# Kernel optimization log

Measured on AMD Instinct MI355X. Metric: run time of the kernel, lower is better.

## Reference

```python
import jax, jax.numpy as jnp
import numpy as np

EPS_RMS = 1e-6  # mmfreelm RMSNorm default eps

def _rmsnorm(x, w):
    var = jnp.mean(x * x, axis=-1, keepdims=True)
    return x * jax.lax.rsqrt(var + EPS_RMS) * w

def _activation_quant(x):
    # per-token absmax int8 quant (BitNet b1.58 activation quant)
    scale = 127.0 / jnp.clip(jnp.max(jnp.abs(x), axis=-1, keepdims=True), 1e-5)
    return jnp.clip(jnp.round(x * scale), -128.0, 127.0) / scale

def _weight_quant(w):
    # ternary quant with global mean-abs scale
    scale = 1.0 / jnp.clip(jnp.mean(jnp.abs(w)), 1e-5)
    return jnp.clip(jnp.round(w * scale), -1.0, 1.0) / scale

def _nm_mask(w, n, m):
    # keep top-n by |w| in every group of m along the input (last) dim
    O, I = w.shape
    g = jnp.abs(w).reshape(-1, m)            # [G, m]
    _, idx = jax.lax.top_k(g, n)             # [G, n]
    rows = jnp.arange(g.shape[0])[:, None]
    mask = jnp.zeros_like(g).at[rows, idx].set(1.0)
    return mask.reshape(O, I)

def setup_inputs() -> dict:
    key = jax.random.key(0)
    k1, k2 = jax.random.split(key)
    B, S, IN, OUT = 4, 2048, 4096, 11008
    x = jax.random.normal(k1, (B, S, IN), dtype=jnp.float32)
    weight = jax.random.normal(k2, (OUT, IN), dtype=jnp.float32) * 0.02
    norm_weight = jnp.ones((IN,), dtype=jnp.float32)
    return {"x": x, "weight": weight, "norm_weight": norm_weight,
            "sparse_n": 2, "sparse_m": 4}

def reference(x, weight, norm_weight, sparse_n, sparse_m):
    x_norm = _rmsnorm(x, norm_weight)
    # STE quantization (forward value == quantized value)
    x_q = x_norm + jax.lax.stop_gradient(_activation_quant(x_norm) - x_norm)
    w_q = weight + jax.lax.stop_gradient(_weight_quant(weight) - weight)
    mask = jax.lax.stop_gradient(_nm_mask(w_q, sparse_n, sparse_m))
    w_sparse = w_q * mask                    # [OUT, IN]
    return jnp.einsum('bsi,oi->bso', x_q, w_sparse)
```

## Files before the change

### kernel.cpp

```cpp
#include <hip/hip_runtime.h>
#include <stdint.h>

#define IN_DIM 4096
#define OUT_DIM 11008
#define TOKENS 8192
#define WN (45088768L)

typedef int int4v __attribute__((ext_vector_type(4)));

__device__ __forceinline__ float bf2f(uint32_t u16) {
  union { uint32_t i; float f; } v; v.i = u16 << 16; return v.f;
}
__device__ __forceinline__ bool probe_bf16(const void* nw) {
  return ((const uint16_t*)nw)[0] == 0x3F80u;
}

__global__ __launch_bounds__(256) void k_wabs(const void* __restrict__ wv,
                                              const void* __restrict__ nwv,
                                              double* __restrict__ partial) {
  const bool b16 = probe_bf16(nwv);
  const long tid = (long)blockIdx.x * 256 + threadIdx.x;
  const long stride = (long)gridDim.x * 256;
  double s = 0.0;
  if (b16) {
    const uint4* w = (const uint4*)wv;
    for (long i = tid; i < WN / 8; i += stride) {
      uint4 v = w[i];
      uint32_t a[4] = {v.x, v.y, v.z, v.w};
      float t = 0.f;
#pragma unroll
      for (int j = 0; j < 4; j++)
        t += fabsf(bf2f(a[j] & 0xffffu)) + fabsf(bf2f(a[j] >> 16));
      s += (double)t;
    }
  } else {
    const float4* w = (const float4*)wv;
    for (long i = tid; i < WN / 4; i += stride) {
      float4 v = w[i];
      s += (double)(fabsf(v.x) + fabsf(v.y) + fabsf(v.z) + fabsf(v.w));
    }
  }
#pragma unroll
  for (int off = 32; off > 0; off >>= 1) s += __shfl_down(s, off);
  __shared__ double sd[4];
  if ((threadIdx.x & 63) == 0) sd[threadIdx.x >> 6] = s;
  __syncthreads();
  if (threadIdx.x == 0) partial[blockIdx.x] = (sd[0] + sd[1]) + (sd[2] + sd[3]);
}

__global__ __launch_bounds__(256) void k_wscale(const double* __restrict__ partial,
                                                float* __restrict__ hdr) {
  double s = 0.0;
  for (int i = threadIdx.x; i < 2048; i += 256) s += partial[i];
#pragma unroll
  for (int off = 32; off > 0; off >>= 1) s += __shfl_down(s, off);
  __shared__ double sd[4];
  if ((threadIdx.x & 63) == 0) sd[threadIdx.x >> 6] = s;
  __syncthreads();
  if (threadIdx.x == 0) {
    double mean = ((sd[0] + sd[1]) + (sd[2] + sd[3])) / (double)WN;
    float meanc = (float)mean;
    if (meanc < 1e-5f) meanc = 1e-5f;
    float wscale = 1.0f / meanc;
    hdr[0] = wscale;
    hdr[1] = 1.0f / wscale;
  }
}

__global__ __launch_bounds__(256) void k_act(const void* __restrict__ xv,
                                             const void* __restrict__ nwv,
                                             int8_t* __restrict__ qx,
                                             float* __restrict__ invsx) {
  const bool b16 = probe_bf16(nwv);
  const int t = blockIdx.x;
  const int tx = threadIdx.x;
  float xw[16];
  float ss = 0.f, mx = 0.f;
  if (b16) {
    const uint16_t* xr = (const uint16_t*)xv + (long)t * IN_DIM;
    const uint16_t* nw = (const uint16_t*)nwv;
#pragma unroll
    for (int c = 0; c < 2; c++) {
      uint4 vx = ((const uint4*)xr)[tx * 2 + c];
      uint4 vn = ((const uint4*)nw)[tx * 2 + c];
      uint32_t ax[4] = {vx.x, vx.y, vx.z, vx.w};
      uint32_t an[4] = {vn.x, vn.y, vn.z, vn.w};
#pragma unroll
      for (int j = 0; j < 4; j++) {
        float x0 = bf2f(ax[j] & 0xffffu), x1 = bf2f(ax[j] >> 16);
        float n0 = bf2f(an[j] & 0xffffu), n1 = bf2f(an[j] >> 16);
        ss += x0 * x0 + x1 * x1;
        float p0 = x0 * n0, p1 = x1 * n1;
        xw[c * 8 + j * 2]     = p0;
        xw[c * 8 + j * 2 + 1] = p1;
        mx = fmaxf(mx, fmaxf(fabsf(p0), fabsf(p1)));
      }
    }
  } else {
    const float* xr = (const float*)xv + (long)t * IN_DIM;
    const float* nw = (const float*)nwv;
#pragma unroll
    for (int c = 0; c < 4; c++) {
      float4 vx = ((const float4*)xr)[tx * 4 + c];
      float4 vn = ((const float4*)nw)[tx * 4 + c];
      ss += vx.x * vx.x + vx.y * vx.y + vx.z * vx.z + vx.w * vx.w;
      float p0 = vx.x * vn.x, p1 = vx.y * vn.y, p2 = vx.z * vn.z, p3 = vx.w * vn.w;
      xw[c * 4 + 0] = p0; xw[c * 4 + 1] = p1; xw[c * 4 + 2] = p2; xw[c * 4 + 3] = p3;
      mx = fmaxf(mx, fmaxf(fmaxf(fabsf(p0), fabsf(p1)), fmaxf(fabsf(p2), fabsf(p3))));
    }
  }
#pragma unroll
  for (int off = 32; off > 0; off >>= 1) {
    ss += __shfl_down(ss, off);
    mx = fmaxf(mx, __shfl_down(mx, off));
  }
  __shared__ float s_ss[4], s_mx[4];
  __shared__ float bc[1];
  if ((tx & 63) == 0) { s_ss[tx >> 6] = ss; s_mx[tx >> 6] = mx; }
  __syncthreads();
  if (tx == 0) {
    float sst = (s_ss[0] + s_ss[1]) + (s_ss[2] + s_ss[3]);
    float mxt = fmaxf(fmaxf(s_mx[0], s_mx[1]), fmaxf(s_mx[2], s_mx[3]));
    float var = sst / (float)IN_DIM;
    float rms = 1.0f / sqrtf(var + 1e-6f);
    float amax = rms * mxt;
    if (amax < 1e-5f) amax = 1e-5f;
    float scale = 127.0f / amax;
    bc[0] = rms * scale;
    invsx[t] = 1.0f / scale;
  }
  __syncthreads();
  float rsc = bc[0];
  uint32_t pw[4];
#pragma unroll
  for (int d = 0; d < 4; d++) {
    uint32_t v = 0;
#pragma unroll
    for (int j = 0; j < 4; j++) {
      float q = rintf(xw[d * 4 + j] * rsc);
      q = fminf(fmaxf(q, -128.f), 127.f);
      int qi = (int)q;
      v |= ((uint32_t)(qi & 0xff)) << (8 * j);
    }
    pw[d] = v;
  }
  uint4 st; st.x = pw[0]; st.y = pw[1]; st.z = pw[2]; st.w = pw[3];
  ((uint4*)(qx + (long)t * IN_DIM))[tx] = st;
}

__global__ __launch_bounds__(256) void k_wq(const void* __restrict__ wv,
                                            const void* __restrict__ nwv,
                                            const float* __restrict__ hdr,
                                            int8_t* __restrict__ qw) {
  const bool b16 = probe_bf16(nwv);
  const long i = (long)blockIdx.x * 256 + threadIdx.x;
  const float wscale = hdr[0];
  float f[8];
  if (b16) {
    uint4 v = ((const uint4*)wv)[i];
    uint32_t a[4] = {v.x, v.y, v.z, v.w};
#pragma unroll
    for (int j = 0; j < 4; j++) {
      f[j * 2]     = bf2f(a[j] & 0xffffu);
      f[j * 2 + 1] = bf2f(a[j] >> 16);
    }
  } else {
    float4 v0 = ((const float4*)wv)[i * 2];
    float4 v1 = ((const float4*)wv)[i * 2 + 1];
    f[0] = v0.x; f[1] = v0.y; f[2] = v0.z; f[3] = v0.w;
    f[4] = v1.x; f[5] = v1.y; f[6] = v1.z; f[7] = v1.w;
  }
  int q[8];
#pragma unroll
  for (int j = 0; j < 8; j++) {
    float qf = rintf(f[j] * wscale);
    qf = fminf(fmaxf(qf, -1.f), 1.f);
    q[j] = (int)qf;
  }
#pragma unroll
  for (int g = 0; g < 2; g++) {
    int cnt = 0;
#pragma unroll
    for (int j = 0; j < 4; j++) {
      int idx = g * 4 + j;
      if (q[idx] != 0) { cnt++; if (cnt > 2) q[idx] = 0; }
    }
  }
  uint32_t lo = 0, hi = 0;
#pragma unroll
  for (int j = 0; j < 4; j++) lo |= ((uint32_t)(q[j] & 0xff)) << (8 * j);
#pragma unroll
  for (int j = 0; j < 4; j++) hi |= ((uint32_t)(q[4 + j] & 0xff)) << (8 * j);
  uint2 st; st.x = lo; st.y = hi;
  ((uint2*)qw)[i] = st;
}

__global__ __launch_bounds__(256) void k_gemm(const int8_t* __restrict__ qx,
                                              const int8_t* __restrict__ qw,
                                              const float* __restrict__ invsx,
                                              const float* __restrict__ hdr,
                                              float* __restrict__ out) {
  __shared__ __align__(16) int8_t sA[128 * 64];
  __shared__ __align__(16) int8_t sB[128 * 64];
  const int tx = threadIdx.x;
  const int wave = tx >> 6, lane = tx & 63;
  const int wr = wave >> 1, wc = wave & 1;
  const int m0 = blockIdx.y * 128, n0 = blockIdx.x * 128;

  const int rowA  = tx >> 2;
  const int col16 = (tx & 3) * 16;
  const int8_t* gA = qx + (long)(m0 + rowA) * IN_DIM + col16;
  const int8_t* gB = qw + (long)(n0 + rowA) * IN_DIM + col16;
  int8_t* lA = sA + wave * 1024;
  int8_t* lB = sB + wave * 1024;

  const int kb = (lane >> 4) * 16;
  const int lr = lane & 15;
  const int8_t* pa[4];
  const int8_t* pb[4];
#pragma unroll
  for (int m = 0; m < 4; m++) pa[m] = sA + (wr * 64 + m * 16 + lr) * 64 + kb;
#pragma unroll
  for (int n = 0; n < 4; n++) pb[n] = sB + (wc * 64 + n * 16 + lr) * 64 + kb;

  int4v zero = {0, 0, 0, 0};
  int4v acc[4][4];
#pragma unroll
  for (int m = 0; m < 4; m++)
#pragma unroll
    for (int n = 0; n < 4; n++) acc[m][n] = zero;

  for (int kt = 0; kt < IN_DIM; kt += 64) {
#pragma unroll
    for (int ph = 0; ph < 2; ph++) {
      __builtin_amdgcn_global_load_lds(
          (const __attribute__((address_space(1))) void*)(gA + (long)ph * 64 * IN_DIM + kt),
          (__attribute__((address_space(3))) void*)(lA + ph * 4096), 16, 0, 0);
      __builtin_amdgcn_global_load_lds(
          (const __attribute__((address_space(1))) void*)(gB + (long)ph * 64 * IN_DIM + kt),
          (__attribute__((address_space(3))) void*)(lB + ph * 4096), 16, 0, 0);
    }
    __syncthreads();
    int4v a[4], b[4];
#pragma unroll
    for (int m = 0; m < 4; m++) a[m] = *(const int4v*)pa[m];
#pragma unroll
    for (int n = 0; n < 4; n++) b[n] = *(const int4v*)pb[n];
#pragma unroll
    for (int m = 0; m < 4; m++)
#pragma unroll
      for (int n = 0; n < 4; n++)
        acc[m][n] = __builtin_amdgcn_mfma_i32_16x16x64_i8(a[m], b[n], acc[m][n], 0, 0, 0);
    __syncthreads();
  }

  const float winv = hdr[1];
#pragma unroll
  for (int m = 0; m < 4; m++) {
    const int rbase = m0 + wr * 64 + m * 16 + (lane >> 4) * 4;
#pragma unroll
    for (int r = 0; r < 4; r++) {
      const int trow = rbase + r;
      const float fs = invsx[trow] * winv;
      const long ob = (long)trow * OUT_DIM + n0 + wc * 64 + lr;
#pragma unroll
      for (int n = 0; n < 4; n++) {
        out[ob + n * 16] = (float)acc[m][n][r] * fs;
      }
    }
  }
}

extern "C" void kernel_launch(void* const* d_in, const int* in_sizes, int n_in,
                              void* d_out, int out_size, void* d_ws, size_t ws_size,
                              hipStream_t stream) {
  const void* x  = d_in[0];
  const void* w  = d_in[1];
  const void* nw = d_in[2];
  float* out = (float*)d_out;

  char* ws = (char*)d_ws;
  float*  hdr     = (float*)ws;
  double* partial = (double*)(ws + 1024);
  float*  invsx   = (float*)(ws + 20480);
  int8_t* qx      = (int8_t*)(ws + (1L << 20));
  int8_t* qw      = (int8_t*)(ws + 36L * (1L << 20));

  hipLaunchKernelGGL(k_wabs,   dim3(2048),   dim3(256), 0, stream, w, nw, partial);
  hipLaunchKernelGGL(k_wscale, dim3(1),      dim3(256), 0, stream, partial, hdr);
  hipLaunchKernelGGL(k_act,    dim3(TOKENS), dim3(256), 0, stream, x, nw, qx, invsx);
  hipLaunchKernelGGL(k_wq,     dim3(22016),  dim3(256), 0, stream, w, nw, hdr, qw);
  hipLaunchKernelGGL(k_gemm,   dim3(OUT_DIM / 128, TOKENS / 128), dim3(256), 0, stream,
                     qx, qw, invsx, hdr, out);
}
```

Baseline: 634.8 us.

## Restructure int8 GEMM with 256x256 tiles, 4-stage LDS pipeline and swizzles

The int8 MFMA GEMM moves from 128x128 tiles with 256 threads and two barriers per k-step to 256x256 tiles with 512 threads. Global-to-LDS loads are issued three stages ahead into a 4-buffer ring, with explicit vmcnt waits and a single barrier per step. An XOR swizzle is applied to LDS columns to avoid bank conflicts, and the block index is remapped for L2 locality. The goal is to hide load latency and raise arithmetic intensity. The cost is 128KB of LDS per block and more accumulator registers, which may limit occupancy despite launch_bounds(512,2).

Result: slower. 716.1 us (+12.8%).

```diff
diff --git a/kernel.cpp b/kernel.cpp
--- a/kernel.cpp
+++ b/kernel.cpp
@@ -5,6 +5,7 @@
 #define OUT_DIM 11008
 #define TOKENS 8192
 #define WN (45088768L)
+#define NKT 64
 
 typedef int int4v __attribute__((ext_vector_type(4)));
 
@@ -195,77 +196,105 @@
   ((uint2*)qw)[i] = st;
 }
 
-__global__ __launch_bounds__(256) void k_gemm(const int8_t* __restrict__ qx,
-                                              const int8_t* __restrict__ qw,
-                                              const float* __restrict__ invsx,
-                                              const float* __restrict__ hdr,
-                                              float* __restrict__ out) {
-  __shared__ __align__(16) int8_t sA[128 * 64];
-  __shared__ __align__(16) int8_t sB[128 * 64];
+__global__ __launch_bounds__(512, 2) void k_gemm(const int8_t* __restrict__ qx,
+                                                 const int8_t* __restrict__ qw,
+                                                 const float* __restrict__ invsx,
+                                                 const float* __restrict__ hdr,
+                                                 float* __restrict__ out) {
+  __shared__ __align__(16) int8_t sA[4][256 * 64];
+  __shared__ __align__(16) int8_t sB[4][256 * 64];
+
   const int tx = threadIdx.x;
   const int wave = tx >> 6, lane = tx & 63;
-  const int wr = wave >> 1, wc = wave & 1;
-  const int m0 = blockIdx.y * 128, n0 = blockIdx.x * 128;
-
-  const int rowA  = tx >> 2;
-  const int col16 = (tx & 3) * 16;
-  const int8_t* gA = qx + (long)(m0 + rowA) * IN_DIM + col16;
-  const int8_t* gB = qw + (long)(n0 + rowA) * IN_DIM + col16;
-  int8_t* lA = sA + wave * 1024;
-  int8_t* lB = sB + wave * 1024;
-
-  const int kb = (lane >> 4) * 16;
+  const int wr = wave >> 2, wc = wave & 3;
   const int lr = lane & 15;
-  const int8_t* pa[4];
-  const int8_t* pb[4];
-#pragma unroll
-  for (int m = 0; m < 4; m++) pa[m] = sA + (wr * 64 + m * 16 + lr) * 64 + kb;
-#pragma unroll
-  for (int n = 0; n < 4; n++) pb[n] = sB + (wc * 64 + n * 16 + lr) * 64 + kb;
-
-  int4v zero = {0, 0, 0, 0};
-  int4v acc[4][4];
-#pragma unroll
-  for (int m = 0; m < 4; m++)
-#pragma unroll
-    for (int n = 0; n < 4; n++) acc[m][n] = zero;
-
-  for (int kt = 0; kt < IN_DIM; kt += 64) {
-#pragma unroll
-    for (int ph = 0; ph < 2; ph++) {
-      __builtin_amdgcn_global_load_lds(
-          (const __attribute__((address_space(1))) void*)(gA + (long)ph * 64 * IN_DIM + kt),
-          (__attribute__((address_space(3))) void*)(lA + ph * 4096), 16, 0, 0);
-      __builtin_amdgcn_global_load_lds(
-          (const __attribute__((address_space(1))) void*)(gB + (long)ph * 64 * IN_DIM + kt),
-          (__attribute__((address_space(3))) void*)(lB + ph * 4096), 16, 0, 0);
-    }
-    __syncthreads();
-    int4v a[4], b[4];
-#pragma unroll
-    for (int m = 0; m < 4; m++) a[m] = *(const int4v*)pa[m];
-#pragma unroll
-    for (int n = 0; n < 4; n++) b[n] = *(const int4v*)pb[n];
-#pragma unroll
-    for (int m = 0; m < 4; m++)
-#pragma unroll
-      for (int n = 0; n < 4; n++)
-        acc[m][n] = __builtin_amdgcn_mfma_i32_16x16x64_i8(a[m], b[n], acc[m][n], 0, 0, 0);
-    __syncthreads();
-  }
+  const int sl = lane >> 4;
+
+  const int bid = blockIdx.x;
+  const int swz = (bid & 7) * 172 + (bid >> 3);
+  const int bm = swz & 31;
+  const int bn = swz >> 5;
+  const int m0 = bm * 256, n0 = bn * 256;
+
+  const int srow  = tx >> 2;
+  const int scol  = ((tx & 3) ^ ((tx >> 3) & 3)) * 16;
+  const int8_t* gA = qx + (long)(m0 + srow) * IN_DIM + scol;
+  const int8_t* gB = qw + (long)(n0 + srow) * IN_DIM + scol;
+
+  auto STAGE = [&](int t) {
+    const int b = t & 3;
+    const long ko = (long)t * 64;
+    __builtin_amdgcn_global_load_lds(
+        (const __attribute__((address_space(1))) void*)(gA + ko),
+        (__attribute__((address_space(3))) void*)(&sA[b][wave * 1024]), 16, 0, 0);
+    __builtin_amdgcn_global_load_lds(
+        (const __attribute__((address_space(1))) void*)(gA + ko + 128L * IN_DIM),
+        (__attribute__((address_space(3))) void*)(&sA[b][8192 + wave * 1024]), 16, 0, 0);
+    __builtin_amdgcn_global_load_lds(
+        (const __attribute__((address_space(1))) void*)(gB + ko),
+        (__attribute__((address_space(3))) void*)(&sB[b][wave * 1024]), 16, 0, 0);
+    __builtin_amdgcn_global_load_lds(
+        (const __attribute__((address_space(1))) void*)(gB + ko + 128L * IN_DIM),
+        (__attribute__((address_space(3))) void*)(&sB[b][8192 + wave * 1024]), 16, 0, 0);
+  };
+
+  int offA[8], offB[4];
+#pragma unroll
+  for (int mi = 0; mi < 8; mi++) {
+    const int row = wr * 128 + mi * 16 + lr;
+    offA[mi] = row * 64 + ((sl ^ ((row >> 1) & 3)) * 16);
+  }
+#pragma unroll
+  for (int ni = 0; ni < 4; ni++) {
+    const int row = wc * 64 + ni * 16 + lr;
+    offB[ni] = row * 64 + ((sl ^ ((row >> 1) & 3)) * 16);
+  }
+
+  int4v acc[8][4];
+#pragma unroll
+  for (int mi = 0; mi < 8; mi++)
+#pragma unroll
+    for (int ni = 0; ni < 4; ni++) { acc[mi][ni][0] = 0; acc[mi][ni][1] = 0; acc[mi][ni][2] = 0; acc[mi][ni][3] = 0; }
+
+  STAGE(0); STAGE(1); STAGE(2);
+
+#define TILE_BODY(T, WAITINSN)                                          \
+  {                                                                     \
+    asm volatile(WAITINSN ::: "memory");                                \
+    __builtin_amdgcn_s_barrier();                                       \
+    __builtin_amdgcn_sched_barrier(0);                                  \
+    const int b_ = (T) & 3;                                             \
+    if ((T) + 3 < NKT) STAGE((T) + 3);                                  \
+    int4v a_[8], bb_[4];                                                \
+    _Pragma("unroll") for (int mi = 0; mi < 8; ++mi)                    \
+        a_[mi] = *(const int4v*)(&sA[b_][offA[mi]]);                    \
+    _Pragma("unroll") for (int ni = 0; ni < 4; ++ni)                    \
+        bb_[ni] = *(const int4v*)(&sB[b_][offB[ni]]);                   \
+    __builtin_amdgcn_s_setprio(1);                                      \
+    _Pragma("unroll") for (int mi = 0; mi < 8; ++mi)                    \
+      _Pragma("unroll") for (int ni = 0; ni < 4; ++ni)                  \
+          acc[mi][ni] = __builtin_amdgcn_mfma_i32_16x16x64_i8(          \
+              a_[mi], bb_[ni], acc[mi][ni], 0, 0, 0);                   \
+    __builtin_amdgcn_s_setprio(0);                                      \
+  }
+
+  for (int t = 0; t < NKT - 2; ++t) TILE_BODY(t, "s_waitcnt vmcnt(8)");
+  TILE_BODY(NKT - 2, "s_waitcnt vmcnt(4)");
+  TILE_BODY(NKT - 1, "s_waitcnt vmcnt(0)");
+#undef TILE_BODY
 
   const float winv = hdr[1];
 #pragma unroll
-  for (int m = 0; m < 4; m++) {
-    const int rbase = m0 + wr * 64 + m * 16 + (lane >> 4) * 4;
+  for (int mi = 0; mi < 8; mi++) {
+    const int rbase = m0 + wr * 128 + mi * 16 + (lane >> 4) * 4;
 #pragma unroll
     for (int r = 0; r < 4; r++) {
       const int trow = rbase + r;
       const float fs = invsx[trow] * winv;
       const long ob = (long)trow * OUT_DIM + n0 + wc * 64 + lr;
 #pragma unroll
-      for (int n = 0; n < 4; n++) {
-        out[ob + n * 16] = (float)acc[m][n][r] * fs;
+      for (int ni = 0; ni < 4; ni++) {
+        out[ob + ni * 16] = (float)acc[mi][ni][r] * fs;
       }
     }
   }
@@ -290,6 +319,6 @@
   hipLaunchKernelGGL(k_wscale, dim3(1),      dim3(256), 0, stream, partial, hdr);
   hipLaunchKernelGGL(k_act,    dim3(TOKENS), dim3(256), 0, stream, x, nw, qx, invsx);
   hipLaunchKernelGGL(k_wq,     dim3(22016),  dim3(256), 0, stream, w, nw, hdr, qw);
-  hipLaunchKernelGGL(k_gemm,   dim3(OUT_DIM / 128, TOKENS / 128), dim3(256), 0, stream,
+  hipLaunchKernelGGL(k_gemm,   dim3(32 * 43), dim3(512), 0, stream,
                      qx, qw, invsx, hdr, out);
 }
```

## Rewrite int8 GEMM with 256x256 tiles, double-buffered LDS pipeline and swizzles

Applied to the files above, without the earlier changes.

The int8 MFMA GEMM moves from 128x128 tiles with 4 waves to 256x256 tiles with 8 waves and a 128-deep K step. It double-buffers LDS, interleaving async global-to-LDS loads for the next tiles with MFMA phases, using explicit waitcnt, barriers and setprio. It also XOR-swizzles LDS columns to avoid bank conflicts and remaps block IDs for L2 locality. The goal is to hide load latency and raise data reuse, at the cost of heavy register use (128 accumulator VGPRs per lane) and 128 KB of LDS per block, which limits occupancy.

Result: faster. 611.8 us (-3.6%).

```diff
diff --git a/kernel.cpp b/kernel.cpp
--- a/kernel.cpp
+++ b/kernel.cpp
@@ -5,8 +5,11 @@
 #define OUT_DIM 11008
 #define TOKENS 8192
 #define WN (45088768L)
+#define NKT128 32
 
 typedef int int4v __attribute__((ext_vector_type(4)));
+#define AS1 __attribute__((address_space(1)))
+#define AS3 __attribute__((address_space(3)))
 
 __device__ __forceinline__ float bf2f(uint32_t u16) {
   union { uint32_t i; float f; } v; v.i = u16 << 16; return v.f;
@@ -195,77 +198,187 @@
   ((uint2*)qw)[i] = st;
 }
 
-__global__ __launch_bounds__(256) void k_gemm(const int8_t* __restrict__ qx,
-                                              const int8_t* __restrict__ qw,
-                                              const float* __restrict__ invsx,
-                                              const float* __restrict__ hdr,
-                                              float* __restrict__ out) {
-  __shared__ __align__(16) int8_t sA[128 * 64];
-  __shared__ __align__(16) int8_t sB[128 * 64];
+__global__ __launch_bounds__(512, 2) void k_gemm(const int8_t* __restrict__ qx,
+                                                 const int8_t* __restrict__ qw,
+                                                 const float* __restrict__ invsx,
+                                                 const float* __restrict__ hdr,
+                                                 float* __restrict__ out) {
+  __shared__ __align__(16) int8_t sA[2][256 * 128];
+  __shared__ __align__(16) int8_t sB[2][256 * 128];
+
   const int tx = threadIdx.x;
   const int wave = tx >> 6, lane = tx & 63;
-  const int wr = wave >> 1, wc = wave & 1;
-  const int m0 = blockIdx.y * 128, n0 = blockIdx.x * 128;
-
-  const int rowA  = tx >> 2;
-  const int col16 = (tx & 3) * 16;
-  const int8_t* gA = qx + (long)(m0 + rowA) * IN_DIM + col16;
-  const int8_t* gB = qw + (long)(n0 + rowA) * IN_DIM + col16;
-  int8_t* lA = sA + wave * 1024;
-  int8_t* lB = sB + wave * 1024;
-
-  const int kb = (lane >> 4) * 16;
-  const int lr = lane & 15;
-  const int8_t* pa[4];
-  const int8_t* pb[4];
-#pragma unroll
-  for (int m = 0; m < 4; m++) pa[m] = sA + (wr * 64 + m * 16 + lr) * 64 + kb;
-#pragma unroll
-  for (int n = 0; n < 4; n++) pb[n] = sB + (wc * 64 + n * 16 + lr) * 64 + kb;
-
-  int4v zero = {0, 0, 0, 0};
-  int4v acc[4][4];
-#pragma unroll
-  for (int m = 0; m < 4; m++)
-#pragma unroll
-    for (int n = 0; n < 4; n++) acc[m][n] = zero;
-
-  for (int kt = 0; kt < IN_DIM; kt += 64) {
-#pragma unroll
-    for (int ph = 0; ph < 2; ph++) {
+  const int wr = wave >> 2, wc = wave & 3;
+  const int fr = lane & 15;
+  const int fg = lane >> 4;
+
+  const int bid = blockIdx.x;
+  const int swz = (bid & 7) * 172 + (bid >> 3);
+  const int m0 = (swz & 31) * 256;
+  const int n0 = (swz >> 5) * 256;
+
+  const int srow = tx >> 3;
+  const int scol = ((tx & 7) ^ ((tx >> 4) & 7)) * 16;
+  const int8_t* gA = qx + (long)(m0 + srow) * IN_DIM + scol;
+  const int8_t* gB = qw + (long)(n0 + srow) * IN_DIM + scol;
+  int8_t* const sA0 = &sA[0][0];
+  int8_t* const sB0 = &sB[0][0];
+
+  auto stageA = [&](int t, int half) {
+    if (t >= NKT128) return;
+    int8_t* base = sA0 + (t & 1) * (256 * 128);
+#pragma unroll
+    for (int l = 0; l < 2; ++l) {
+      const int rb = half * 128 + l * 64;
       __builtin_amdgcn_global_load_lds(
-          (const __attribute__((address_space(1))) void*)(gA + (long)ph * 64 * IN_DIM + kt),
-          (__attribute__((address_space(3))) void*)(lA + ph * 4096), 16, 0, 0);
+          (const AS1 void*)(gA + (long)t * 128 + (long)rb * IN_DIM),
+          (AS3 void*)(base + rb * 128 + wave * 1024), 16, 0, 0);
+    }
+  };
+  auto stageB = [&](int t, int half) {
+    if (t >= NKT128) return;
+    int8_t* base = sB0 + (t & 1) * (256 * 128);
+#pragma unroll
+    for (int l = 0; l < 2; ++l) {
+      const int rb = half * 128 + l * 64;
       __builtin_amdgcn_global_load_lds(
-          (const __attribute__((address_space(1))) void*)(gB + (long)ph * 64 * IN_DIM + kt),
-          (__attribute__((address_space(3))) void*)(lB + ph * 4096), 16, 0, 0);
-    }
-    __syncthreads();
-    int4v a[4], b[4];
-#pragma unroll
-    for (int m = 0; m < 4; m++) a[m] = *(const int4v*)pa[m];
-#pragma unroll
-    for (int n = 0; n < 4; n++) b[n] = *(const int4v*)pb[n];
-#pragma unroll
-    for (int m = 0; m < 4; m++)
-#pragma unroll
-      for (int n = 0; n < 4; n++)
-        acc[m][n] = __builtin_amdgcn_mfma_i32_16x16x64_i8(a[m], b[n], acc[m][n], 0, 0, 0);
-    __syncthreads();
+          (const AS1 void*)(gB + (long)t * 128 + (long)rb * IN_DIM),
+          (AS3 void*)(base + rb * 128 + wave * 1024), 16, 0, 0);
+    }
+  };
+
+  int offA[8][2], offB[4][2];
+#pragma unroll
+  for (int mi = 0; mi < 8; ++mi) {
+    const int row = wr * 128 + mi * 16 + fr;
+    const int xr = (row >> 1) & 7;
+#pragma unroll
+    for (int ks = 0; ks < 2; ++ks)
+      offA[mi][ks] = row * 128 + (((ks * 4 + fg) ^ xr) * 16);
+  }
+#pragma unroll
+  for (int ni = 0; ni < 4; ++ni) {
+    const int row = wc * 64 + ni * 16 + fr;
+    const int xr = (row >> 1) & 7;
+#pragma unroll
+    for (int ks = 0; ks < 2; ++ks)
+      offB[ni][ks] = row * 128 + (((ks * 4 + fg) ^ xr) * 16);
+  }
+
+  int4v acc[8][4];
+#pragma unroll
+  for (int mi = 0; mi < 8; ++mi)
+#pragma unroll
+    for (int ni = 0; ni < 4; ++ni) {
+      acc[mi][ni][0] = 0; acc[mi][ni][1] = 0; acc[mi][ni][2] = 0; acc[mi][ni][3] = 0;
+    }
+
+  stageA(0, 0); stageA(0, 1); stageB(0, 0); stageB(0, 1);
+  stageA(1, 0); stageA(1, 1);
+  asm volatile("s_waitcnt vmcnt(4)" ::: "memory");
+  __builtin_amdgcn_s_barrier();
+
+  int4v a[8][2];
+  int4v bf[2][2];
+
+#pragma unroll 2
+  for (int t = 0; t < NKT128; ++t) {
+    const int bofs = (t & 1) * (256 * 128);
+
+#pragma unroll
+    for (int j = 0; j < 2; ++j) {
+      bf[j][0] = *(const int4v*)(sB0 + bofs + offB[j][0]);
+      bf[j][1] = *(const int4v*)(sB0 + bofs + offB[j][1]);
+    }
+#pragma unroll
+    for (int mi = 0; mi < 4; ++mi) {
+      a[mi][0] = *(const int4v*)(sA0 + bofs + offA[mi][0]);
+      a[mi][1] = *(const int4v*)(sA0 + bofs + offA[mi][1]);
+    }
+    stageB(t + 1, 0);
+    asm volatile("s_waitcnt lgkmcnt(8)" ::: "memory");
+    __builtin_amdgcn_s_barrier();
+    asm volatile("s_waitcnt lgkmcnt(0)" ::: "memory");
+    __builtin_amdgcn_s_setprio(1);
+#pragma unroll
+    for (int mi = 0; mi < 4; ++mi)
+#pragma unroll
+      for (int j = 0; j < 2; ++j)
+#pragma unroll
+        for (int ks = 0; ks < 2; ++ks)
+          acc[mi][j] = __builtin_amdgcn_mfma_i32_16x16x64_i8(a[mi][ks], bf[j][ks], acc[mi][j], 0, 0, 0);
+    __builtin_amdgcn_s_setprio(0);
+    __builtin_amdgcn_s_barrier();
+
+#pragma unroll
+    for (int mi = 4; mi < 8; ++mi) {
+      a[mi][0] = *(const int4v*)(sA0 + bofs + offA[mi][0]);
+      a[mi][1] = *(const int4v*)(sA0 + bofs + offA[mi][1]);
+    }
+    stageB(t + 1, 1);
+    __builtin_amdgcn_s_barrier();
+    asm volatile("s_waitcnt lgkmcnt(0)" ::: "memory");
+    __builtin_amdgcn_s_setprio(1);
+#pragma unroll
+    for (int mi = 4; mi < 8; ++mi)
+#pragma unroll
+      for (int j = 0; j < 2; ++j)
+#pragma unroll
+        for (int ks = 0; ks < 2; ++ks)
+          acc[mi][j] = __builtin_amdgcn_mfma_i32_16x16x64_i8(a[mi][ks], bf[j][ks], acc[mi][j], 0, 0, 0);
+    __builtin_amdgcn_s_setprio(0);
+    __builtin_amdgcn_s_barrier();
+
+#pragma unroll
+    for (int j = 0; j < 2; ++j) {
+      bf[j][0] = *(const int4v*)(sB0 + bofs + offB[2 + j][0]);
+      bf[j][1] = *(const int4v*)(sB0 + bofs + offB[2 + j][1]);
+    }
+    stageA(t + 2, 0);
+    __builtin_amdgcn_s_barrier();
+    asm volatile("s_waitcnt lgkmcnt(0)" ::: "memory");
+    __builtin_amdgcn_s_setprio(1);
+#pragma unroll
+    for (int mi = 0; mi < 4; ++mi)
+#pragma unroll
+      for (int j = 0; j < 2; ++j)
+#pragma unroll
+        for (int ks = 0; ks < 2; ++ks)
+          acc[mi][2 + j] = __builtin_amdgcn_mfma_i32_16x16x64_i8(a[mi][ks], bf[j][ks], acc[mi][2 + j], 0, 0, 0);
+    __builtin_amdgcn_s_setprio(0);
+    __builtin_amdgcn_s_barrier();
+
+    stageA(t + 2, 1);
+    if (t < NKT128 - 2) {
+      asm volatile("s_waitcnt vmcnt(4)" ::: "memory");
+    } else {
+      asm volatile("s_waitcnt vmcnt(0)" ::: "memory");
+    }
+    __builtin_amdgcn_s_barrier();
+    __builtin_amdgcn_s_setprio(1);
+#pragma unroll
+    for (int mi = 4; mi < 8; ++mi)
+#pragma unroll
+      for (int j = 0; j < 2; ++j)
+#pragma unroll
+        for (int ks = 0; ks < 2; ++ks)
+          acc[mi][2 + j] = __builtin_amdgcn_mfma_i32_16x16x64_i8(a[mi][ks], bf[j][ks], acc[mi][2 + j], 0, 0, 0);
+    __builtin_amdgcn_s_setprio(0);
+    __builtin_amdgcn_s_barrier();
   }
 
   const float winv = hdr[1];
 #pragma unroll
-  for (int m = 0; m < 4; m++) {
-    const int rbase = m0 + wr * 64 + m * 16 + (lane >> 4) * 4;
-#pragma unroll
-    for (int r = 0; r < 4; r++) {
+  for (int mi = 0; mi < 8; ++mi) {
+    const int rbase = m0 + wr * 128 + mi * 16 + (lane >> 4) * 4;
+#pragma unroll
+    for (int r = 0; r < 4; ++r) {
       const int trow = rbase + r;
       const float fs = invsx[trow] * winv;
-      const long ob = (long)trow * OUT_DIM + n0 + wc * 64 + lr;
-#pragma unroll
-      for (int n = 0; n < 4; n++) {
-        out[ob + n * 16] = (float)acc[m][n][r] * fs;
+      const long ob = (long)trow * OUT_DIM + n0 + wc * 64 + fr;
+#pragma unroll
+      for (int ni = 0; ni < 4; ++ni) {
+        out[ob + ni * 16] = (float)acc[mi][ni][r] * fs;
       }
     }
   }
@@ -290,6 +403,6 @@
   hipLaunchKernelGGL(k_wscale, dim3(1),      dim3(256), 0, stream, partial, hdr);
   hipLaunchKernelGGL(k_act,    dim3(TOKENS), dim3(256), 0, stream, x, nw, qx, invsx);
   hipLaunchKernelGGL(k_wq,     dim3(22016),  dim3(256), 0, stream, w, nw, hdr, qw);
-  hipLaunchKernelGGL(k_gemm,   dim3(OUT_DIM / 128, TOKENS / 128), dim3(256), 0, stream,
+  hipLaunchKernelGGL(k_gemm,   dim3(32 * 43), dim3(512), 0, stream,
                      qx, qw, invsx, hdr, out);
 }
```
